# Optimization experiments

Hardware: AMD Instinct MI355X
Metric: run time of the kernel (lower is better)

The kernel has to match this reference:

```python
import jax, jax.numpy as jnp
import numpy as np
from math import factorial

N_SCALES = 4
K_ORI = 4
NA = 9


def _grids(h, w):
    fy = (jnp.arange(h) - h // 2) * (2.0 / h)
    fx = (jnp.arange(w) - w // 2) * (2.0 / w)
    FY, FX = jnp.meshgrid(fy, fx, indexing='ij')
    r = jnp.sqrt(FX ** 2 + FY ** 2)
    r = jnp.where(r == 0, 1.0 / max(h, w), r)
    return jnp.log2(r), jnp.arctan2(FY, FX)


def _rc_hi(lr, lo, hi):
    # sqrt raised-cosine rising 0->1 over log_rad in [lo, hi]
    t = jnp.clip((lr - lo) / (hi - lo), 0.0, 1.0)
    return jnp.sqrt(0.5 * (1.0 - jnp.cos(jnp.pi * t)))


def _rc_lo(lr, lo, hi):
    t = jnp.clip((lr - lo) / (hi - lo), 0.0, 1.0)
    return jnp.sqrt(0.5 * (1.0 + jnp.cos(jnp.pi * t)))


def _angle_masks(angle, K, is_complex):
    order = K - 1
    const = (2.0 ** (2 * order)) * (factorial(order) ** 2) / (K * factorial(2 * order))
    masks = []
    for b in range(K):
        d = jnp.mod(angle - jnp.pi * b / K + jnp.pi, 2 * jnp.pi) - jnp.pi
        if is_complex:  # single-sided (analytic) mask
            m = 2.0 * np.sqrt(const) * (jnp.cos(d) ** order) * (jnp.abs(d) < jnp.pi / 2)
        else:
            m = np.sqrt(const) * (jnp.cos(d) ** order)
        masks.append(m)
    return masks


def _build_pyramid(img, n_scales, K):
    # complex steerable pyramid in the frequency domain (tight_frame=False)
    order = K - 1
    h, w = img.shape
    imdft = jnp.fft.fftshift(jnp.fft.fft2(img))
    lr, ang = _grids(h, w)
    hi0 = _rc_hi(lr, -1.0, 0.0)
    lo0 = _rc_lo(lr, -1.0, 0.0)
    coeffs = {'residual_highpass': jnp.real(jnp.fft.ifft2(jnp.fft.ifftshift(imdft * hi0)))}
    lodft = imdft * lo0
    cph = (-1j) ** order
    for s in range(n_scales):
        hh, ww = lodft.shape
        lr, ang = _grids(hh, ww)
        him = _rc_hi(lr, -2.0, -1.0)
        for b, am in enumerate(_angle_masks(ang, K, True)):
            coeffs[(s, b)] = jnp.fft.ifft2(jnp.fft.ifftshift(cph * lodft * him * am))
        # spectral crop = spatial downsample by 2, then lowpass
        lodft = lodft[hh // 4: hh // 4 + hh // 2, ww // 4: ww // 4 + ww // 2]
        lr2, _ = _grids(hh // 2, ww // 2)
        lodft = lodft * _rc_lo(lr2, -1.0, 0.0)
    coeffs['residual_lowpass'] = jnp.real(jnp.fft.ifft2(jnp.fft.ifftshift(lodft)))
    return coeffs


def _lo0_filter(im):
    # height-0 pyramid residual lowpass == lo0 filtering (filterPyr in the torch code)
    h, w = im.shape
    lr, _ = _grids(h, w)
    return jnp.real(jnp.fft.ifft2(jnp.fft.ifftshift(jnp.fft.fftshift(jnp.fft.fft2(im)) * _rc_lo(lr, -1.0, 0.0))))


def _expand(im, f=2):
    # frequency-domain upsampling by factor f (Portilla_Simoncelli.expand)
    h, w = im.shape
    dft = jnp.fft.fftshift(jnp.fft.fft2(im)).astype(jnp.complex64)
    big = jnp.zeros((f * h, f * w), dtype=jnp.complex64)
    big = big.at[(f * h - h) // 2:(f * h - h) // 2 + h, (f * w - w) // 2:(f * w - w) // 2 + w].set(dft)
    return jnp.fft.ifft2(jnp.fft.ifftshift(big)) * (f * f)


def _recon_band(real_bands, K):
    # recon_pyr(levels=[0]) of a height-1 real pyramid whose bands were replaced
    order = K - 1
    h, w = real_bands[0].shape
    lr, ang = _grids(h, w)
    lo0 = _rc_lo(lr, -1.0, 0.0)
    him = _rc_hi(lr, -2.0, -1.0)
    ph = (1j) ** order
    recondft = jnp.zeros((h, w), dtype=jnp.complex64)
    for b, am in enumerate(_angle_masks(ang, K, False)):
        recondft = recondft + ph * jnp.fft.fftshift(jnp.fft.fft2(real_bands[b])) * him * am
    return jnp.real(jnp.fft.ifft2(jnp.fft.ifftshift(recondft * lo0)))


def _autocorr(ch, la):
    h, w = ch.shape
    F = jnp.fft.fft2(ch)
    ac = jnp.fft.fftshift(jnp.real(jnp.fft.ifft2(jnp.abs(F) ** 2))) / (h * w)
    cx, cy = h // 2, w // 2
    le = int(min(min(h, w) / 2 - 1, la))
    return ac[cx - le:cx + le + 1, cy - le:cy + le + 1], ac[cx, cy], le


def _skew_kurt(ch, vari, var0):
    cond = (vari / var0) > 1e-6
    skew = jnp.where(cond, jnp.mean(ch ** 3) / (vari ** 1.5), 0.0)
    kurt = jnp.where(cond, jnp.mean(ch ** 4) / (vari ** 2), 3.0)
    return skew, kurt


def _ps_forward(image):
    n_scales, K, Na = N_SCALES, K_ORI, NA
    img = image.reshape(image.shape[-2], image.shape[-1])
    mu = jnp.mean(img)
    var0 = jnp.var(img, ddof=1)
    cimg = img - mu
    pix = jnp.stack([mu, var0,
                     jnp.mean(cimg ** 3) / (var0 ** 1.5),
                     jnp.mean(cimg ** 4) / (var0 ** 2),
                     jnp.min(img), jnp.max(img)])
    coeffs = _build_pyramid(img, n_scales, K)
    coeffs['residual_lowpass'] = coeffs['residual_lowpass'] - jnp.mean(coeffs['residual_lowpass'])
    keys = ['residual_highpass'] + [(s, b) for s in range(n_scales) for b in range(K)] + ['residual_lowpass']
    mag, realc, mag_means = {}, {}, []
    for kk in keys:
        v = coeffs[kk]
        m = jnp.abs(v)
        mm = jnp.mean(m)
        mag_means.append(mm)
        mag[kk] = m - mm
        realc[kk] = jnp.real(v)
    mag_means = jnp.stack(mag_means)
    la = (Na - 1) // 2
    auto_corr = jnp.zeros((Na, Na, n_scales + 1))
    acm = jnp.zeros((Na, Na, n_scales, K))
    skew_r = jnp.zeros((n_scales + 1,))
    kurt_r = jnp.zeros((n_scales + 1,))
    recon = _lo0_filter(coeffs['residual_lowpass'])
    patch, vari, le = _autocorr(recon, la)
    auto_corr = auto_corr.at[la - le:la + le + 1, la - le:la + le + 1, n_scales].set(patch)
    sk, ku = _skew_kurt(recon, vari, var0)
    skew_r = skew_r.at[n_scales].set(sk)
    kurt_r = kurt_r.at[n_scales].set(ku)
    for s in range(n_scales - 1, -1, -1):
        for b in range(K):
            patch, vari, le = _autocorr(mag[(s, b)], la)
            acm = acm.at[la - le:la + le + 1, la - le:la + le + 1, s, b].set(patch)
        recon = jnp.real(_expand(recon, 2) / 4.0)
        recon = recon + _recon_band([realc[(s, b)] for b in range(K)], K)
        patch, vari, le = _autocorr(recon, la)
        auto_corr = auto_corr.at[la - le:la + le + 1, la - le:la + le + 1, s].set(patch)
        sk, ku = _skew_kurt(recon, vari, var0)
        skew_r = skew_r.at[s].set(sk)
        kurt_r = kurt_r.at[s].set(ku)
    K2 = max(2 * K, 5)
    coc_mag = jnp.zeros((K, K, n_scales + 1))
    csc_mag = jnp.zeros((K, K, n_scales))
    coc_real = jnp.zeros((K2, K2, n_scales + 1))
    csc_real = jnp.zeros((2 * K, K2, n_scales))
    for s in range(n_scales):
        hs, ws = realc[(s, 0)].shape
        csz = hs * ws
        if s < n_scales - 1:
            pars, rpr, rpi = [], [], []
            for b in range(K):
                tmp = _expand(coeffs[(s + 1, b)], 2) / 4.0
                rt, it = jnp.real(tmp), jnp.imag(tmp)
                mg = jnp.sqrt(rt ** 2 + it ** 2)
                a2 = 2.0 * jnp.arctan2(rt, it)  # note arg order matches torch code
                rpr.append((mg * jnp.cos(a2)).T.reshape(-1))
                rpi.append((mg * jnp.sin(a2)).T.reshape(-1))
                pars.append((mg - jnp.mean(mg)).T.reshape(-1))
            parents = jnp.stack(pars, 1)
            rparents = jnp.stack(rpr + rpi, 1)
        else:
            tmp = jnp.real(_expand(coeffs['residual_lowpass'], 2) / 4.0).T
            rparents = jnp.stack([tmp.reshape(-1),
                                  jnp.roll(tmp, 1, 0).reshape(-1),
                                  jnp.roll(tmp, -1, 0).reshape(-1),
                                  jnp.roll(tmp, 1, 1).reshape(-1),
                                  jnp.roll(tmp, -1, 1).reshape(-1)], 1)
            parents = None
        cousins = jnp.stack([mag[(s, b)].T.reshape(-1) for b in range(K)], 1)
        coc_mag = coc_mag.at[:, :, s].set(cousins.T @ cousins / csz)
        if parents is not None:
            csc_mag = csc_mag.at[:, :, s].set(cousins.T @ parents / csz)
        rcousins = jnp.stack([realc[(s, b)].T.reshape(-1) for b in range(K)], 1)
        coc_real = coc_real.at[:K, :K, s].set(rcousins.T @ rcousins / csz)
        nrp = rparents.shape[1]
        csc_real = csc_real.at[:K, :nrp, s].set(rcousins.T @ rparents / csz)
        if s == n_scales - 1:
            coc_real = coc_real.at[:nrp, :nrp, n_scales].set(rparents.T @ rparents / (csz / 4.0))
    var_hp = jnp.mean(coeffs['residual_highpass'] ** 2)
    return jnp.concatenate([pix, mag_means, acm.reshape(-1), skew_r, kurt_r,
                            auto_corr.reshape(-1), coc_mag.reshape(-1), csc_mag.reshape(-1),
                            coc_real.reshape(-1), csc_real.reshape(-1), var_hp.reshape(1)])


def setup_inputs() -> dict:
    key = jax.random.key(0)
    image = jax.random.normal(key, (1, 1, 1024, 1024), dtype=jnp.float32)
    return {"image": image}


def reference(image):
    return _ps_forward(image)
```

## Files before the change

kernel.cpp:

```cpp
#include <hip/hip_runtime.h>
#include <math.h>

typedef float2 cplx;

#define PI_F 3.14159265358979323846f
#define SQC  0.8944271909999159f

#define GS_FOR(i, n) for (int i = blockIdx.x * blockDim.x + threadIdx.x; i < (n); i += gridDim.x * blockDim.x)
#define RED_GRID 256

__device__ __forceinline__ float ufreq(int i, int n) {
  return (float)((i < (n >> 1)) ? i : i - n) * (2.0f / (float)n);
}
__device__ __forceinline__ void grid_lr_ang(int i, int j, int n, float* lr, float* ang) {
  float fy = ufreq(i, n), fx = ufreq(j, n);
  float r = sqrtf(fx * fx + fy * fy);
  if (i == 0 && j == 0) r = 1.0f / (float)n;
  *lr = log2f(r);
  *ang = atan2f(fy, fx);
}
__device__ __forceinline__ float rc_hi_f(float lr, float lo, float hi) {
  float t = (lr - lo) / (hi - lo);
  t = fminf(fmaxf(t, 0.0f), 1.0f);
  return sqrtf(0.5f * (1.0f - cosf(PI_F * t)));
}
__device__ __forceinline__ float rc_lo_f(float lr, float lo, float hi) {
  float t = (lr - lo) / (hi - lo);
  t = fminf(fmaxf(t, 0.0f), 1.0f);
  return sqrtf(0.5f * (1.0f + cosf(PI_F * t)));
}
__device__ __forceinline__ float wrap_d(float ang, int b) {
  float d = ang - PI_F * (float)b * 0.25f + PI_F;
  d = d - floorf(d * (0.5f / PI_F)) * (2.0f * PI_F);
  return d - PI_F;
}
__device__ __forceinline__ float amask_c(float ang, int b) {
  float d = wrap_d(ang, b);
  float c = cosf(d);
  float m = 2.0f * SQC * c * c * c;
  return (fabsf(d) < 0.5f * PI_F) ? m : 0.0f;
}
__device__ __forceinline__ float amask_r(float ang, int b) {
  float d = wrap_d(ang, b);
  float c = cosf(d);
  return SQC * c * c * c;
}

__device__ __forceinline__ double wred_d(double v) {
#pragma unroll
  for (int o = 32; o > 0; o >>= 1) v += __shfl_down(v, o);
  return v;
}
template<int NS>
__device__ __forceinline__ void block_to_parts(double* __restrict__ part, int slotBase, double* v) {
  __shared__ double lds[NS][4];
  const int wid = threadIdx.x >> 6, lane = threadIdx.x & 63;
#pragma unroll
  for (int q = 0; q < NS; ++q) {
    double r = wred_d(v[q]);
    if (lane == 0) lds[q][wid] = r;
  }
  __syncthreads();
  for (int q = threadIdx.x; q < NS; q += blockDim.x) {
    double s = lds[q][0] + lds[q][1] + lds[q][2] + lds[q][3];
    part[(size_t)(slotBase + q) * RED_GRID + blockIdx.x] = s;
  }
}
__global__ void reduce_parts_k(double* __restrict__ acc, const double* __restrict__ part, int base) {
  const double* p = part + (size_t)(base + blockIdx.x) * RED_GRID;
  double s = 0;
  for (int i = threadIdx.x; i < RED_GRID; i += 64) s += p[i];
  s = wred_d(s);
  if (threadIdx.x == 0) acc[base + blockIdx.x] = s;
}
__device__ __forceinline__ void atomicMinF(float* a, float v) {
  if (v >= 0.0f) atomicMin((int*)a, __float_as_int(v));
  else atomicMax((unsigned int*)a, __float_as_uint(v));
}
__device__ __forceinline__ void atomicMaxF(float* a, float v) {
  if (v >= 0.0f) atomicMax((int*)a, __float_as_int(v));
  else atomicMin((unsigned int*)a, __float_as_uint(v));
}

template<int LOGN, bool INV>
__global__ __launch_bounds__(256) void fft_rows_k(cplx* __restrict__ d) {
  constexpr int N = 1 << LOGN;
  __shared__ cplx sh[N];
  __shared__ cplx tw[N / 2];
  const int tid = threadIdx.x;
  const int T = blockDim.x;
  cplx* rp = d + (size_t)blockIdx.x * N;
  for (int k = tid; k < N / 2; k += T) {
    float a = (INV ? 2.0f : -2.0f) * PI_F * (float)k / (float)N;
    float s, c;
    sincosf(a, &s, &c);
    tw[k] = make_float2(c, s);
  }
  for (int i = tid; i < N; i += T) {
    unsigned r = __brev((unsigned)i) >> (32 - LOGN);
    sh[r] = rp[i];
  }
  __syncthreads();
  for (int len = 2; len <= N; len <<= 1) {
    const int half = len >> 1;
    const int tstep = N / len;
    for (int j = tid; j < N / 2; j += T) {
      int pos = j & (half - 1);
      int base = (j - pos) << 1;
      cplx w = tw[pos * tstep];
      cplx a = sh[base + pos];
      cplx b = sh[base + pos + half];
      float tx = b.x * w.x - b.y * w.y;
      float ty = b.x * w.y + b.y * w.x;
      sh[base + pos] = make_float2(a.x + tx, a.y + ty);
      sh[base + pos + half] = make_float2(a.x - tx, a.y - ty);
    }
    __syncthreads();
  }
  const float sc = INV ? (1.0f / (float)N) : 1.0f;
  for (int i = tid; i < N; i += T) {
    cplx v = sh[i];
    rp[i] = make_float2(v.x * sc, v.y * sc);
  }
}

__global__ void transpose_k(cplx* __restrict__ out, const cplx* __restrict__ in, int N) {
  __shared__ cplx tile[32][33];
  size_t po = (size_t)blockIdx.z * N * N;
  int bx = blockIdx.x * 32, by = blockIdx.y * 32;
  int x = bx + threadIdx.x;
  for (int dy = threadIdx.y; dy < 32; dy += 8)
    tile[dy][threadIdx.x] = in[po + (size_t)(by + dy) * N + x];
  __syncthreads();
  int xo = by + threadIdx.x;
  for (int dy = threadIdx.y; dy < 32; dy += 8)
    out[po + (size_t)(bx + dy) * N + xo] = tile[threadIdx.x][dy];
}

__global__ void r2c_k(cplx* out, const float* in, int n) {
  GS_FOR(i, n) out[i] = make_float2(in[i], 0.0f);
}
__global__ void hp_lo_split_k(cplx* hp, cplx* lod, const cplx* spec, int logN) {
  int N = 1 << logN, n = N * N;
  GS_FOR(idx, n) {
    int i = idx >> logN, j = idx & (N - 1);
    float lr, ang;
    grid_lr_ang(i, j, N, &lr, &ang);
    float h0 = rc_hi_f(lr, -1.0f, 0.0f);
    float l0 = rc_lo_f(lr, -1.0f, 0.0f);
    cplx z = spec[idx];
    hp[idx]  = make_float2(z.x * h0, z.y * h0);
    lod[idx] = make_float2(z.x * l0, z.y * l0);
  }
}
__global__ void rhp_stats_k(const cplx* src, int n, double* part) {
  double sa = 0, sq = 0;
  GS_FOR(i, n) {
    float v = src[i].x;
    sa += fabsf(v);
    sq += (double)v * (double)v;
  }
  double v[2] = {sa, sq};
  block_to_parts<2>(part, 4, v);
}
__global__ void band_spec_k(cplx* out, const cplx* lod, int logN, int b0, int P) {
  int N = 1 << logN, n = N * N;
  GS_FOR(idx, n) {
    int i = idx >> logN, j = idx & (N - 1);
    float lr, ang;
    grid_lr_ang(i, j, N, &lr, &ang);
    float him = rc_hi_f(lr, -2.0f, -1.0f);
    cplx z = lod[idx];
    for (int p = 0; p < P; ++p) {
      float m = him * amask_c(ang, b0 + p);
      out[p * n + idx] = make_float2(-z.y * m, z.x * m);
    }
  }
}
template<int P>
__global__ void extract_band_k(float* realc, float* mag, const cplx* src, int logPer,
                               double* part, int slotBase) {
  int n = (1 << logPer) * P;
  double s0 = 0, s1 = 0, s2 = 0, s3 = 0;
  GS_FOR(idx, n) {
    cplx z = src[idx];
    float m = sqrtf(z.x * z.x + z.y * z.y);
    realc[idx] = z.x;
    mag[idx] = m;
    int p = idx >> logPer;
    if (p == 0) s0 += m; else if (p == 1) s1 += m; else if (p == 2) s2 += m; else s3 += m;
  }
  double v[4] = {s0, s1, s2, s3};
  block_to_parts<P>(part, slotBase, v);
}
__global__ void center_k(float* buf, int logPer, int P, const double* acc0) {
  int nPer = 1 << logPer, n = nPer * P;
  double inv = 1.0 / (double)nPer;
  GS_FOR(idx, n) buf[idx] -= (float)(acc0[idx >> logPer] * inv);
}
__global__ void lod_down_k(cplx* child, const cplx* par, int logNc) {
  int Nc = 1 << logNc, n = Nc * Nc, Np = Nc << 1;
  GS_FOR(idx, n) {
    int i = idx >> logNc, j = idx & (Nc - 1);
    int pi = (i < (Nc >> 1)) ? i : i + Nc;
    int pj = (j < (Nc >> 1)) ? j : j + Nc;
    float lr, ang;
    grid_lr_ang(i, j, Nc, &lr, &ang);
    float l0 = rc_lo_f(lr, -1.0f, 0.0f);
    cplx z = par[pi * Np + pj];
    child[idx] = make_float2(z.x * l0, z.y * l0);
  }
}
__global__ void sum_real2_k(const cplx* src, int n, double* part) {
  double s = 0;
  GS_FOR(i, n) s += (double)src[i].x;
  double v[1] = {s};
  block_to_parts<1>(part, 24, v);
}
__global__ void center_abs2_k(const cplx* src, int n, const double* acc, double* part) {
  float mu = (float)(acc[24] / (double)n);
  double s = 0;
  GS_FOR(i, n) s += fabsf(src[i].x - mu);
  double v[1] = {s};
  block_to_parts<1>(part, 25, v);
}
__global__ void rs4_init_k(cplx* rs, const cplx* lod4) {
  GS_FOR(idx, 4096) {
    int i = idx >> 6, j = idx & 63;
    float lr, ang;
    grid_lr_ang(i, j, 64, &lr, &ang);
    float l0 = rc_lo_f(lr, -1.0f, 0.0f);
    cplx v = lod4[idx];
    if (idx == 0) v = make_float2(0.0f, 0.0f);
    rs[idx] = make_float2(v.x * l0, v.y * l0);
  }
}
__global__ void embed_rs_k(cplx* dst, const cplx* src, int logNb, int zeroDC) {
  int Nb = 1 << logNb, Nc = Nb >> 1, q = Nc >> 1, n = Nb * Nb;
  GS_FOR(idx, n) {
    int i = idx >> logNb, j = idx & (Nb - 1);
    int ci = (i < q) ? i : ((i >= Nb - q) ? (i - Nb + Nc) : -1);
    int cj = (j < q) ? j : ((j >= Nb - q) ? (j - Nb + Nc) : -1);
    cplx v = make_float2(0.0f, 0.0f);
    if (ci >= 0 && cj >= 0) {
      v = src[ci * Nc + cj];
      if (zeroDC && ci == 0 && cj == 0) v = make_float2(0.0f, 0.0f);
    }
    dst[idx] = v;
  }
}
__global__ void recon_accum_k(cplx* rs, const cplx* lod, int logN) {
  int N = 1 << logN, n = N * N;
  GS_FOR(idx, n) {
    int i = idx >> logN, j = idx & (N - 1);
    int ni = (N - i) & (N - 1), nj = (N - j) & (N - 1);
    float lr, ang;
    grid_lr_ang(i, j, N, &lr, &ang);
    float him = rc_hi_f(lr, -2.0f, -1.0f);
    float l0 = rc_lo_f(lr, -1.0f, 0.0f);
    cplx L = lod[idx];
    cplx L2 = lod[ni * N + nj];
    float sx = 0.0f, sy = 0.0f;
#pragma unroll
    for (int b = 0; b < 4; ++b) {
      float c1 = him * amask_c(ang, b);
      float c2 = him * amask_c(ang + PI_F, b);
      float mr = him * amask_r(ang, b);
      float gx = L.x * c1 - L2.x * c2;
      float gy = L.y * c1 + L2.y * c2;
      sx += 0.5f * mr * gx;
      sy += 0.5f * mr * gy;
    }
    cplx prev = rs[idx];
    rs[idx] = make_float2(prev.x + sx * l0, prev.y + sy * l0);
  }
}
__global__ void embed_band_k(cplx* dst, const cplx* lodc, int logNb, int b0, int P) {
  int Nb = 1 << logNb, Nc = Nb >> 1, q = Nc >> 1, n = Nb * Nb;
  int tot = n * P;
  GS_FOR(idxAll, tot) {
    int p = idxAll >> (2 * logNb);
    int idx = idxAll & (n - 1);
    int i = idx >> logNb, j = idx & (Nb - 1);
    int ci = (i < q) ? i : ((i >= Nb - q) ? (i - Nb + Nc) : -1);
    int cj = (j < q) ? j : ((j >= Nb - q) ? (j - Nb + Nc) : -1);
    cplx v = make_float2(0.0f, 0.0f);
    if (ci >= 0 && cj >= 0) {
      float lr, ang;
      grid_lr_ang(ci, cj, Nc, &lr, &ang);
      float m = rc_hi_f(lr, -2.0f, -1.0f) * amask_c(ang, b0 + p);
      cplx z = lodc[ci * Nc + cj];
      v = make_float2(-z.y * m, z.x * m);
    }
    dst[idxAll] = v;
  }
}
template<int ST, bool SK>
__global__ void ac_spatial_k(const float* __restrict__ x, int logN, double* part, int slotBase0) {
  constexpr int NS = SK ? 43 : 41;
  const int N = 1 << logN;
  const int n = N * N;
  const int p = blockIdx.y;
  const float* xp = x + (((size_t)p << (2 * logN)) * ST);
  float acc[41];
#pragma unroll
  for (int q = 0; q < 41; ++q) acc[q] = 0.0f;
  float a3 = 0.0f, a4 = 0.0f;
  for (int idx = blockIdx.x * blockDim.x + threadIdx.x; idx < n; idx += gridDim.x * blockDim.x) {
    int i = idx >> logN, j = idx & (N - 1);
    float xc = xp[(size_t)idx * ST];
    if (SK) {
      float x2 = xc * xc;
      a3 += x2 * xc;
      a4 += x2 * x2;
    }
#pragma unroll
    for (int q = 0; q < 41; ++q) {
      const int di = (q < 5) ? 0 : 1 + (q - 5) / 9;
      const int dj = (q < 5) ? q : ((q - 5) % 9) - 4;
      int i2 = (i + di) & (N - 1);
      int j2 = (j + dj) & (N - 1);
      acc[q] += xc * xp[(size_t)((i2 << logN) | j2) * ST];
    }
  }
  double v[NS];
#pragma unroll
  for (int q = 0; q < 41; ++q) v[q] = (double)acc[q];
  if (SK) { v[41] = (double)a3; v[42] = (double)a4; }
  block_to_parts<NS>(part, slotBase0 + p * NS, v);
}
__global__ void img_stats1_k(const float* img, int n, double* part, float* mm) {
  double s = 0;
  float mn = INFINITY, mx = -INFINITY;
  GS_FOR(i, n) {
    float v = img[i];
    s += (double)v;
    mn = fminf(mn, v);
    mx = fmaxf(mx, v);
  }
  double v[1] = {s};
  block_to_parts<1>(part, 0, v);
#pragma unroll
  for (int o = 32; o > 0; o >>= 1) {
    mn = fminf(mn, __shfl_down(mn, o));
    mx = fmaxf(mx, __shfl_down(mx, o));
  }
  if ((threadIdx.x & 63) == 0) {
    atomicMinF(mm + 0, mn);
    atomicMaxF(mm + 1, mx);
  }
}
__global__ void img_stats2_k(const float* img, int n, const double* acc, double* part) {
  double mu = acc[0] / (double)n;
  double s2 = 0, s3 = 0, s4 = 0;
  GS_FOR(i, n) {
    double c = (double)img[i] - mu;
    double c2 = c * c;
    s2 += c2;
    s3 += c2 * c;
    s4 += c2 * c2;
  }
  double v[3] = {s2, s3, s4};
  block_to_parts<3>(part, 1, v);
}
template<bool WS>
__global__ void gram4_k(const float* base, int n, double* part, int slotBase) {
  constexpr int NS = WS ? 20 : 16;
  double g[16];
  double s[4];
#pragma unroll
  for (int q = 0; q < 16; ++q) g[q] = 0;
#pragma unroll
  for (int q = 0; q < 4; ++q) s[q] = 0;
  GS_FOR(i, n) {
    double d0 = base[i], d1 = base[n + i], d2 = base[2 * n + i], d3 = base[3 * n + i];
    g[0] += d0 * d0; g[1] += d0 * d1; g[2]  += d0 * d2; g[3]  += d0 * d3;
    g[5] += d1 * d1; g[6] += d1 * d2; g[7]  += d1 * d3;
    g[10] += d2 * d2; g[11] += d2 * d3;
    g[15] += d3 * d3;
    if (WS) { s[0] += d0; s[1] += d1; s[2] += d2; s[3] += d3; }
  }
  g[4] = g[1]; g[8] = g[2]; g[12] = g[3]; g[9] = g[6]; g[13] = g[7]; g[14] = g[11];
  double v[NS];
#pragma unroll
  for (int q = 0; q < 16; ++q) v[q] = g[q];
  if (WS) {
#pragma unroll
    for (int q = 0; q < 4; ++q) v[16 + q] = s[q];
  }
  block_to_parts<NS>(part, slotBase, v);
}
__global__ void parent_reduce_k(const cplx* par, const float* magS, const float* realS, int n,
                                double* part, int slotBase) {
  double d[13];
#pragma unroll
  for (int q = 0; q < 13; ++q) d[q] = 0;
  GS_FOR(i, n) {
    cplx z = par[i];
    float rt = z.x, it = z.y;
    float mg = sqrtf(rt * rt + it * it);
    float rpr = 0.0f, rpi = 0.0f;
    if (mg > 0.0f) {
      rpr = (it * it - rt * rt) / mg;
      rpi = 2.0f * rt * it / mg;
    }
    d[0] += (double)mg;
#pragma unroll
    for (int b = 0; b < 4; ++b) d[1 + b] += (double)magS[b * n + i] * (double)mg;
#pragma unroll
    for (int b = 0; b < 4; ++b) {
      double rv = (double)realS[b * n + i];
      d[5 + b] += rv * (double)rpr;
      d[9 + b] += rv * (double)rpi;
    }
  }
  block_to_parts<13>(part, slotBase, d);
}
__global__ void lp_parent2_k(const cplx* X, const float* realS, int logN, double* part) {
  int N = 1 << logN, n = N * N;
  double d[45];
#pragma unroll
  for (int q = 0; q < 45; ++q) d[q] = 0;
  GS_FOR(idx, n) {
    int i = idx >> logN, j = idx & (N - 1);
    float c[5];
    c[0] = X[idx].x;
    c[1] = X[i * N + ((j - 1) & (N - 1))].x;
    c[2] = X[i * N + ((j + 1) & (N - 1))].x;
    c[3] = X[((i - 1) & (N - 1)) * N + j].x;
    c[4] = X[((i + 1) & (N - 1)) * N + j].x;
#pragma unroll
    for (int b = 0; b < 4; ++b) {
      double rv = (double)realS[b * n + idx];
#pragma unroll
      for (int k = 0; k < 5; ++k) d[b * 5 + k] += rv * (double)c[k];
    }
#pragma unroll
    for (int a = 0; a < 5; ++a)
#pragma unroll
      for (int k = 0; k < 5; ++k) d[20 + a * 5 + k] += (double)c[a] * (double)c[k];
  }
  block_to_parts<45>(part, 370, d);
}
__global__ void init_mm_k(float* mm) {
  if (threadIdx.x == 0) { mm[0] = INFINITY; mm[1] = -INFINITY; }
}

__global__ void assemble_k(float* out, const double* acc, const float* mm) {
  const int t = threadIdx.x;
  const double NPIX = 1048576.0;
  double var0 = acc[1] / (NPIX - 1.0);
  if (t == 0) {
    double mu = acc[0] / NPIX;
    out[0] = (float)mu;
    out[1] = (float)var0;
    out[2] = (float)((acc[2] / NPIX) / pow(var0, 1.5));
    out[3] = (float)((acc[3] / NPIX) / (var0 * var0));
    out[4] = mm[0];
    out[5] = mm[1];
    out[2455] = (float)(acc[5] / NPIX);
  }
  for (int k = t; k < 18; k += blockDim.x) {
    double n, sv;
    if (k == 0) { n = NPIX; sv = acc[4]; }
    else if (k == 17) { n = 4096.0; sv = acc[25]; }
    else { int s = (k - 1) >> 2; double dd = (double)(1024 >> s); n = dd * dd; sv = acc[7 + k]; }
    out[6 + k] = (float)(sv / n);
  }
  for (int si = t; si < 5; si += blockDim.x) {
    double dd = (si == 4) ? 64.0 : (double)(1024 >> si);
    double nn = dd * dd;
    double vari = acc[1104 + si * 43] / nn;
    bool cond = (vari / var0) > 1e-6;
    double m3 = acc[1104 + si * 43 + 41] / nn, m4 = acc[1104 + si * 43 + 42] / nn;
    out[1320 + si] = (float)(cond ? m3 / pow(vari, 1.5) : 0.0);
    out[1325 + si] = (float)(cond ? m4 / (vari * vari) : 3.0);
  }
  for (int w = t; w < 656; w += blockDim.x) {
    int patch = w / 41, q = w - patch * 41;
    int s = patch >> 2, b = patch & 3;
    double dd = (double)(1024 >> s);
    double v = acc[448 + w] / (dd * dd);
    int di = (q < 5) ? 0 : 1 + (q - 5) / 9;
    int dj = (q < 5) ? q : ((q - 5) % 9) - 4;
    int pi = 4 + di, pj = 4 + dj;
    out[24 + 144 * pi + 16 * pj + 4 * s + b] = (float)v;
    if (q) out[24 + 144 * (8 - pi) + 16 * (8 - pj) + 4 * s + b] = (float)v;
  }
  for (int w = t; w < 205; w += blockDim.x) {
    int si = w / 41, q = w - si * 41;
    double dd = (si == 4) ? 64.0 : (double)(1024 >> si);
    double v = acc[1104 + si * 43 + q] / (dd * dd);
    int di = (q < 5) ? 0 : 1 + (q - 5) / 9;
    int dj = (q < 5) ? q : ((q - 5) % 9) - 4;
    int pi = 4 + di, pj = 4 + dj;
    out[1330 + (pi * 9 + pj) * 5 + si] = (float)v;
    if (q) out[1330 + ((8 - pi) * 9 + (8 - pj)) * 5 + si] = (float)v;
  }
  for (int q = t; q < 64; q += blockDim.x) {
    int s = q >> 4, ij = q & 15;
    double dd = (double)(1024 >> s); double csz = dd * dd;
    out[1735 + ij * 5 + s] = (float)(acc[64 + s * 20 + ij] / csz);
  }
  for (int q = t; q < 64; q += blockDim.x) {
    int s = q >> 4, ij = q & 15;
    int i = ij >> 2, j = ij & 3;
    double dd = (double)(1024 >> s); double csz = dd * dd;
    out[1879 + (i * 8 + j) * 5 + s] = (float)(acc[144 + s * 16 + ij] / csz);
  }
  for (int q = t; q < 25; q += blockDim.x) {
    int a = q / 5, b2 = q - a * 5;
    out[1879 + (a * 8 + b2) * 5 + 4] = (float)(acc[390 + q] / 4096.0);
  }
  for (int q = t; q < 48; q += blockDim.x) {
    int s = q >> 4, ij = q & 15;
    int i = ij >> 2, pb = ij & 3;
    double dd = (double)(1024 >> s); double csz = dd * dd;
    const double* ps = acc + 208 + (s * 4 + pb) * 13;
    double meanp = ps[0] / csz;
    double cousSum = acc[64 + s * 20 + 16 + i];
    out[1815 + (i * 4 + pb) * 4 + s] = (float)((ps[1 + i] - meanp * cousSum) / csz);
  }
  for (int q = t; q < 96; q += blockDim.x) {
    int s = q >> 5, r = q & 31;
    int i = r >> 3, j = r & 7;
    int pb = j & 3, offq = (j >= 4) ? 9 : 5;
    double dd = (double)(1024 >> s); double csz = dd * dd;
    out[2199 + (i * 8 + j) * 4 + s] = (float)(acc[208 + (s * 4 + pb) * 13 + offq + i] / csz);
  }
  for (int q = t; q < 20; q += blockDim.x) {
    int i = q / 5, c = q - i * 5;
    out[2199 + (i * 8 + c) * 4 + 3] = (float)(acc[370 + q] / 16384.0);
  }
}

static void fft_rows(cplx* d, int N, int rows, bool inv, hipStream_t st) {
  dim3 g(rows);
  int T = (N >= 512) ? 256 : ((N == 256) ? 128 : 64);
  dim3 b(T);
  switch (N) {
    case 64:   if (inv) fft_rows_k<6,  true><<<g, b, 0, st>>>(d); else fft_rows_k<6,  false><<<g, b, 0, st>>>(d); break;
    case 128:  if (inv) fft_rows_k<7,  true><<<g, b, 0, st>>>(d); else fft_rows_k<7,  false><<<g, b, 0, st>>>(d); break;
    case 256:  if (inv) fft_rows_k<8,  true><<<g, b, 0, st>>>(d); else fft_rows_k<8,  false><<<g, b, 0, st>>>(d); break;
    case 512:  if (inv) fft_rows_k<9,  true><<<g, b, 0, st>>>(d); else fft_rows_k<9,  false><<<g, b, 0, st>>>(d); break;
    case 1024: if (inv) fft_rows_k<10, true><<<g, b, 0, st>>>(d); else fft_rows_k<10, false><<<g, b, 0, st>>>(d); break;
    default: break;
  }
}
static void fft2d(cplx* a, cplx* b, int N, int P, bool inv, hipStream_t st) {
  fft_rows(a, N, N * P, inv, st);
  dim3 tg(N / 32, N / 32, P), tb(32, 8);
  transpose_k<<<tg, tb, 0, st>>>(b, a, N);
  fft_rows(b, N, N * P, inv, st);
  transpose_k<<<tg, tb, 0, st>>>(a, b, N);
}
static inline dim3 gsz(int n) {
  int b = (n + 255) >> 8;
  if (b > 2048) b = 2048;
  if (b < 1) b = 1;
  return dim3(b);
}

extern "C" void kernel_launch(void* const* d_in, const int* in_sizes, int n_in,
                              void* d_out, int out_size, void* d_ws, size_t ws_size,
                              hipStream_t stream) {
  (void)in_sizes; (void)n_in; (void)out_size; (void)ws_size;
  const float* img = (const float*)d_in[0];
  float* out = (float*)d_out;

  char* wsb = (char*)d_ws;
  size_t off = 0;
  auto alloc = [&](size_t bytes) -> void* {
    void* p = wsb + off;
    off += (bytes + 255) & ~(size_t)255;
    return p;
  };
  const size_t MB = (size_t)1 << 20;
  const int NSLOT = 1320;
  cplx* cA = (cplx*)alloc(16 * MB);
  cplx* cB = (cplx*)alloc(16 * MB);
  cplx* LOD[5];
  for (int s = 0; s < 5; ++s) {
    int N = 1024 >> s;
    LOD[s] = (cplx*)alloc((size_t)N * N * sizeof(cplx));
  }
  cplx* RS[4];
  for (int k = 0; k < 4; ++k) {
    int N = 64 << k;
    RS[k] = (cplx*)alloc((size_t)N * N * sizeof(cplx));
  }
  float* MAG[4];
  float* REALC[4];
  for (int s = 0; s < 4; ++s) {
    int N = 1024 >> s;
    MAG[s] = (float*)alloc((size_t)4 * N * N * sizeof(float));
  }
  for (int s = 0; s < 4; ++s) {
    int N = 1024 >> s;
    REALC[s] = (float*)alloc((size_t)4 * N * N * sizeof(float));
  }
  const int NPIX = 1024 * 1024;
  double* PART = (double*)alloc((size_t)NSLOT * RED_GRID * 8);
  double* ACC  = (double*)alloc(2048 * 8);
  float* MM    = (float*)alloc(256);

  auto finish = [&](int base, int count) {
    reduce_parts_k<<<dim3(count), 64, 0, stream>>>(ACC, PART, base);
  };

  hipMemsetAsync(out, 0, 2456 * sizeof(float), stream);
  init_mm_k<<<1, 64, 0, stream>>>(MM);

  img_stats1_k<<<dim3(RED_GRID), 256, 0, stream>>>(img, NPIX, PART, MM);
  finish(0, 1);
  img_stats2_k<<<dim3(RED_GRID), 256, 0, stream>>>(img, NPIX, ACC, PART);

  r2c_k<<<gsz(NPIX), 256, 0, stream>>>(cA, img, NPIX);
  fft2d(cA, cB, 1024, 1, false, stream);
  hp_lo_split_k<<<gsz(NPIX), 256, 0, stream>>>(cA, LOD[0], cA, 10);
  fft2d(cA, cB, 1024, 1, true, stream);
  rhp_stats_k<<<dim3(RED_GRID), 256, 0, stream>>>(cA, NPIX, PART);
  for (int b0 = 0; b0 < 4; b0 += 2) {
    band_spec_k<<<gsz(NPIX), 256, 0, stream>>>(cA, LOD[0], 10, b0, 2);
    fft2d(cA, cB, 1024, 2, true, stream);
    extract_band_k<2><<<dim3(RED_GRID), 256, 0, stream>>>(REALC[0] + (size_t)b0 * NPIX,
                                                          MAG[0] + (size_t)b0 * NPIX, cA, 20, PART, 8 + b0);
  }
  finish(8, 4);
  center_k<<<gsz(4 * NPIX), 256, 0, stream>>>(MAG[0], 20, 4, ACC + 8);
  lod_down_k<<<gsz(512 * 512), 256, 0, stream>>>(LOD[1], LOD[0], 9);
  for (int s = 1; s <= 3; ++s) {
    int N = 1024 >> s, logN = 10 - s, n = N * N;
    band_spec_k<<<gsz(n), 256, 0, stream>>>(cA, LOD[s], logN, 0, 4);
    fft2d(cA, cB, N, 4, true, stream);
    extract_band_k<4><<<dim3(RED_GRID), 256, 0, stream>>>(REALC[s], MAG[s], cA, 2 * logN, PART, 8 + 4 * s);
    finish(8 + 4 * s, 4);
    center_k<<<gsz(4 * n), 256, 0, stream>>>(MAG[s], 2 * logN, 4, ACC + 8 + 4 * s);
    lod_down_k<<<gsz((N / 2) * (N / 2)), 256, 0, stream>>>(LOD[s + 1], LOD[s], logN - 1);
  }
  hipMemcpyAsync(cA, LOD[4], 4096 * sizeof(cplx), hipMemcpyDeviceToDevice, stream);
  fft2d(cA, cB, 64, 1, true, stream);
  sum_real2_k<<<dim3(RED_GRID), 256, 0, stream>>>(cA, 4096, PART);
  finish(24, 1);
  center_abs2_k<<<dim3(RED_GRID), 256, 0, stream>>>(cA, 4096, ACC, PART);

  for (int s = 0; s < 4; ++s) {
    dim3 g(RED_GRID, 4);
    ac_spatial_k<1, false><<<g, 256, 0, stream>>>(MAG[s], 10 - s, PART, 448 + s * 4 * 41);
  }

  rs4_init_k<<<gsz(4096), 256, 0, stream>>>(RS[0], LOD[4]);
  hipMemcpyAsync(cA, RS[0], 4096 * sizeof(cplx), hipMemcpyDeviceToDevice, stream);
  fft2d(cA, cB, 64, 1, true, stream);
  ac_spatial_k<2, true><<<dim3(RED_GRID, 1), 256, 0, stream>>>((const float*)cA, 6, PART, 1104 + 4 * 43);
  cplx* cur = RS[0];
  for (int s = 3; s >= 0; --s) {
    int N = 1024 >> s, logN = 10 - s, n = N * N;
    cplx* nxt = (s > 0) ? RS[4 - s] : cA;
    embed_rs_k<<<gsz(n), 256, 0, stream>>>(nxt, cur, logN, 0);
    recon_accum_k<<<gsz(n), 256, 0, stream>>>(nxt, LOD[s], logN);
    if (s > 0) {
      hipMemcpyAsync(cA, nxt, (size_t)n * sizeof(cplx), hipMemcpyDeviceToDevice, stream);
    }
    fft2d(cA, cB, N, 1, true, stream);
    ac_spatial_k<2, true><<<dim3(RED_GRID, 1), 256, 0, stream>>>((const float*)cA, logN, PART, 1104 + s * 43);
    cur = nxt;
  }

  for (int s = 0; s < 4; ++s) {
    int n = (1024 >> s) * (1024 >> s);
    gram4_k<true><<<dim3(RED_GRID), 256, 0, stream>>>(MAG[s], n, PART, 64 + s * 20);
    gram4_k<false><<<dim3(RED_GRID), 256, 0, stream>>>(REALC[s], n, PART, 144 + s * 16);
  }
  for (int pb0 = 0; pb0 < 4; pb0 += 2) {
    embed_band_k<<<gsz(2 * NPIX), 256, 0, stream>>>(cA, LOD[1], 10, pb0, 2);
    fft2d(cA, cB, 1024, 2, true, stream);
    for (int p = 0; p < 2; ++p)
      parent_reduce_k<<<dim3(RED_GRID), 256, 0, stream>>>(cA + (size_t)p * NPIX, MAG[0], REALC[0], NPIX,
                                                          PART, 208 + (pb0 + p) * 13);
  }
  for (int s = 1; s <= 2; ++s) {
    int N = 1024 >> s, logN = 10 - s, n = N * N;
    embed_band_k<<<gsz(4 * n), 256, 0, stream>>>(cA, LOD[s + 1], logN, 0, 4);
    fft2d(cA, cB, N, 4, true, stream);
    for (int p = 0; p < 4; ++p)
      parent_reduce_k<<<dim3(RED_GRID), 256, 0, stream>>>(cA + (size_t)p * n, MAG[s], REALC[s], n,
                                                          PART, 208 + (s * 4 + p) * 13);
  }
  embed_rs_k<<<gsz(128 * 128), 256, 0, stream>>>(cA, LOD[4], 7, 1);
  fft2d(cA, cB, 128, 1, true, stream);
  lp_parent2_k<<<dim3(RED_GRID), 256, 0, stream>>>(cA, REALC[3], 7, PART);

  finish(0, NSLOT);
  assemble_k<<<1, 256, 0, stream>>>(out, ACC, MM);
}
```

Baseline: 1.226 ms.

## Register-tile spatial autocorrelation, merge scale launches, fuse recon embed with accumulate

The spatial autocorrelation kernel now has each thread handle 8 consecutive pixels. It loads a 5x16 neighbourhood into registers with float4 loads and reuses it for all 41 lag products, where before it did a separate strided load per lag. The four per-scale magnitude autocorrelation launches are folded into one 3D-grid launch, and the embed and recon-accumulate kernels are fused into one kernel that writes the destination once. These changes cut global memory traffic and launch count, at the cost of more registers per thread and possibly lower occupancy.

```diff
diff --git a/kernel.cpp b/kernel.cpp
--- a/kernel.cpp
+++ b/kernel.cpp
@@ -249,17 +249,22 @@
     dst[idx] = v;
   }
 }
-__global__ void recon_accum_k(cplx* rs, const cplx* lod, int logN) {
-  int N = 1 << logN, n = N * N;
+__global__ void recon_step_k(cplx* __restrict__ dst, const cplx* __restrict__ src,
+                             const cplx* __restrict__ lod, int logNb) {
+  int Nb = 1 << logNb, Nc = Nb >> 1, qq = Nc >> 1, n = Nb * Nb;
   GS_FOR(idx, n) {
-    int i = idx >> logN, j = idx & (N - 1);
-    int ni = (N - i) & (N - 1), nj = (N - j) & (N - 1);
+    int i = idx >> logNb, j = idx & (Nb - 1);
+    int ci = (i < qq) ? i : ((i >= Nb - qq) ? (i - Nb + Nc) : -1);
+    int cj = (j < qq) ? j : ((j >= Nb - qq) ? (j - Nb + Nc) : -1);
+    float ex = 0.0f, ey = 0.0f;
+    if (ci >= 0 && cj >= 0) { cplx v = src[ci * Nc + cj]; ex = v.x; ey = v.y; }
+    int ni = (Nb - i) & (Nb - 1), nj = (Nb - j) & (Nb - 1);
     float lr, ang;
-    grid_lr_ang(i, j, N, &lr, &ang);
+    grid_lr_ang(i, j, Nb, &lr, &ang);
     float him = rc_hi_f(lr, -2.0f, -1.0f);
     float l0 = rc_lo_f(lr, -1.0f, 0.0f);
     cplx L = lod[idx];
-    cplx L2 = lod[ni * N + nj];
+    cplx L2 = lod[ni * Nb + nj];
     float sx = 0.0f, sy = 0.0f;
 #pragma unroll
     for (int b = 0; b < 4; ++b) {
@@ -271,8 +276,7 @@
       sx += 0.5f * mr * gx;
       sy += 0.5f * mr * gy;
     }
-    cplx prev = rs[idx];
-    rs[idx] = make_float2(prev.x + sx * l0, prev.y + sy * l0);
+    dst[idx] = make_float2(ex + sx * l0, ey + sy * l0);
   }
 }
 __global__ void embed_band_k(cplx* dst, const cplx* lodc, int logNb, int b0, int P) {
@@ -296,38 +300,69 @@
   }
 }
 template<int ST, bool SK>
-__global__ void ac_spatial_k(const float* __restrict__ x, int logN, double* part, int slotBase0) {
-  constexpr int NS = SK ? 43 : 41;
+__device__ __forceinline__ void ac_core(const float* __restrict__ xp, int logN,
+                                        double* __restrict__ part, int slotBase) {
   const int N = 1 << logN;
-  const int n = N * N;
-  const int p = blockIdx.y;
-  const float* xp = x + (((size_t)p << (2 * logN)) * ST);
+  const int nu = (N * N) >> 3;
   float acc[41];
 #pragma unroll
   for (int q = 0; q < 41; ++q) acc[q] = 0.0f;
   float a3 = 0.0f, a4 = 0.0f;
-  for (int idx = blockIdx.x * blockDim.x + threadIdx.x; idx < n; idx += gridDim.x * blockDim.x) {
-    int i = idx >> logN, j = idx & (N - 1);
-    float xc = xp[(size_t)idx * ST];
-    if (SK) {
-      float x2 = xc * xc;
-      a3 += x2 * xc;
-      a4 += x2 * x2;
-    }
-#pragma unroll
-    for (int q = 0; q < 41; ++q) {
-      const int di = (q < 5) ? 0 : 1 + (q - 5) / 9;
-      const int dj = (q < 5) ? q : ((q - 5) % 9) - 4;
-      int i2 = (i + di) & (N - 1);
-      int j2 = (j + dj) & (N - 1);
-      acc[q] += xc * xp[(size_t)((i2 << logN) | j2) * ST];
-    }
-  }
+  for (int u = blockIdx.x * blockDim.x + threadIdx.x; u < nu; u += gridDim.x * blockDim.x) {
+    int i = u >> (logN - 3);
+    int j0 = (u & ((N >> 3) - 1)) << 3;
+    float buf[5][16];
+#pragma unroll
+    for (int di = 0; di < 5; ++di) {
+      int r = ((i + di) & (N - 1)) << logN;
+#pragma unroll
+      for (int blk = 0; blk < 4; ++blk) {
+        int c = (j0 - 4 + blk * 4) & (N - 1);
+        if (ST == 1) {
+          const float4 v = *reinterpret_cast<const float4*>(xp + r + c);
+          buf[di][blk * 4 + 0] = v.x; buf[di][blk * 4 + 1] = v.y;
+          buf[di][blk * 4 + 2] = v.z; buf[di][blk * 4 + 3] = v.w;
+        } else {
+          const float4 v0 = *reinterpret_cast<const float4*>(xp + ((size_t)(r + c) << 1));
+          const float4 v1 = *reinterpret_cast<const float4*>(xp + ((size_t)(r + c) << 1) + 4);
+          buf[di][blk * 4 + 0] = v0.x; buf[di][blk * 4 + 1] = v0.z;
+          buf[di][blk * 4 + 2] = v1.x; buf[di][blk * 4 + 3] = v1.z;
+        }
+      }
+    }
+#pragma unroll
+    for (int k = 0; k < 8; ++k) {
+      float xc = buf[0][4 + k];
+      if (SK) {
+        float x2 = xc * xc;
+        a3 += x2 * xc;
+        a4 += x2 * x2;
+      }
+#pragma unroll
+      for (int q = 0; q < 41; ++q) {
+        const int di = (q < 5) ? 0 : 1 + (q - 5) / 9;
+        const int dj = (q < 5) ? q : ((q - 5) % 9) - 4;
+        acc[q] += xc * buf[di][4 + k + dj];
+      }
+    }
+  }
+  constexpr int NS = SK ? 43 : 41;
   double v[NS];
 #pragma unroll
   for (int q = 0; q < 41; ++q) v[q] = (double)acc[q];
   if (SK) { v[41] = (double)a3; v[42] = (double)a4; }
-  block_to_parts<NS>(part, slotBase0 + p * NS, v);
+  block_to_parts<NS>(part, slotBase, v);
+}
+__global__ __launch_bounds__(256) void acm_vec_k(const float* m0, const float* m1,
+                                                 const float* m2, const float* m3, double* part) {
+  const int s = blockIdx.z;
+  const float* base = (s == 0) ? m0 : ((s == 1) ? m1 : ((s == 2) ? m2 : m3));
+  const int logN = 10 - s;
+  const float* xp = base + ((size_t)blockIdx.y << (2 * logN));
+  ac_core<1, false>(xp, logN, part, 448 + (s * 4 + blockIdx.y) * 41);
+}
+__global__ __launch_bounds__(256) void ac_rec_k(const float* x, int logN, double* part, int slotBase) {
+  ac_core<2, true>(x, logN, part, slotBase);
 }
 __global__ void img_stats1_k(const float* img, int n, double* part, float* mm) {
   double s = 0;
@@ -644,26 +679,22 @@
   finish(24, 1);
   center_abs2_k<<<dim3(RED_GRID), 256, 0, stream>>>(cA, 4096, ACC, PART);
 
-  for (int s = 0; s < 4; ++s) {
-    dim3 g(RED_GRID, 4);
-    ac_spatial_k<1, false><<<g, 256, 0, stream>>>(MAG[s], 10 - s, PART, 448 + s * 4 * 41);
-  }
+  acm_vec_k<<<dim3(RED_GRID, 4, 4), 256, 0, stream>>>(MAG[0], MAG[1], MAG[2], MAG[3], PART);
 
   rs4_init_k<<<gsz(4096), 256, 0, stream>>>(RS[0], LOD[4]);
   hipMemcpyAsync(cA, RS[0], 4096 * sizeof(cplx), hipMemcpyDeviceToDevice, stream);
   fft2d(cA, cB, 64, 1, true, stream);
-  ac_spatial_k<2, true><<<dim3(RED_GRID, 1), 256, 0, stream>>>((const float*)cA, 6, PART, 1104 + 4 * 43);
+  ac_rec_k<<<dim3(RED_GRID), 256, 0, stream>>>((const float*)cA, 6, PART, 1104 + 4 * 43);
   cplx* cur = RS[0];
   for (int s = 3; s >= 0; --s) {
     int N = 1024 >> s, logN = 10 - s, n = N * N;
     cplx* nxt = (s > 0) ? RS[4 - s] : cA;
-    embed_rs_k<<<gsz(n), 256, 0, stream>>>(nxt, cur, logN, 0);
-    recon_accum_k<<<gsz(n), 256, 0, stream>>>(nxt, LOD[s], logN);
+    recon_step_k<<<gsz(n), 256, 0, stream>>>(nxt, cur, LOD[s], logN);
     if (s > 0) {
       hipMemcpyAsync(cA, nxt, (size_t)n * sizeof(cplx), hipMemcpyDeviceToDevice, stream);
     }
     fft2d(cA, cB, N, 1, true, stream);
-    ac_spatial_k<2, true><<<dim3(RED_GRID, 1), 256, 0, stream>>>((const float*)cA, logN, PART, 1104 + s * 43);
+    ac_rec_k<<<dim3(RED_GRID), 256, 0, stream>>>((const float*)cA, logN, PART, 1104 + s * 43);
     cur = nxt;
   }
 
```

Measured after the change: 1.216 ms. About the same (-0.8%).
